# Kernel tuning notes

Hardware: AMD Instinct MI355X
Metric: run time of the kernel (lower is better)

Reference implementation:

```python
import jax, jax.numpy as jnp
import numpy as np

N = 100000
E = 1600000
F_IN = 512
H1, C1 = 8, 8      # layer-1: 8 heads, 8 dims each (concat -> 64)
H2, C2 = 1, 16     # layer-2: 1 head, num_classes=16
SLOPE = 0.2        # GATConv leaky_relu negative slope


def setup_inputs() -> dict:
    key = jax.random.key(0)
    ks = jax.random.split(key, 10)
    x = jax.random.normal(ks[0], (N, F_IN), dtype=jnp.float32)
    edge_index = jax.random.randint(ks[1], (2, E), 0, N, dtype=jnp.int32)
    s = 0.05
    W1 = jax.random.normal(ks[2], (F_IN, H1 * C1), dtype=jnp.float32) * s
    a1_src = jax.random.normal(ks[3], (H1, C1), dtype=jnp.float32) * s
    a1_dst = jax.random.normal(ks[4], (H1, C1), dtype=jnp.float32) * s
    b1 = jnp.zeros((H1 * C1,), dtype=jnp.float32)
    W2 = jax.random.normal(ks[5], (H1 * C1, H2 * C2), dtype=jnp.float32) * s
    a2_src = jax.random.normal(ks[6], (H2, C2), dtype=jnp.float32) * s
    a2_dst = jax.random.normal(ks[7], (H2, C2), dtype=jnp.float32) * s
    b2 = jnp.zeros((H2 * C2,), dtype=jnp.float32)
    return {"x": x, "edge_index": edge_index, "W1": W1, "a1_src": a1_src,
            "a1_dst": a1_dst, "b1": b1, "W2": W2, "a2_src": a2_src,
            "a2_dst": a2_dst, "b2": b2}


def _gat_conv(h, src, dst, W, a_src, a_dst, b, heads, ch):
    n = h.shape[0]
    hp = (h @ W).reshape(n, heads, ch)                      # [N,H,C]
    al_s = jnp.einsum('nhc,hc->nh', hp, a_src)              # [N,H]
    al_d = jnp.einsum('nhc,hc->nh', hp, a_dst)              # [N,H]
    e = jax.nn.leaky_relu(al_s[src] + al_d[dst], SLOPE)     # [E,H]
    # segment softmax over edges sharing a destination (self-loops guarantee >=1 edge/node)
    emax = jax.lax.stop_gradient(jax.ops.segment_max(e, dst, num_segments=n))
    ee = jnp.exp(e - emax[dst])
    denom = jax.ops.segment_sum(ee, dst, num_segments=n)
    alpha = ee / denom[dst]                                 # [E,H]
    msg = hp[src] * alpha[:, :, None]                       # [E,H,C]
    out = jax.ops.segment_sum(msg, dst, num_segments=n)     # [N,H,C]
    return out.reshape(n, heads * ch) + b


def reference(x, edge_index, W1, a1_src, a1_dst, b1, W2, a2_src, a2_dst, b2):
    n = x.shape[0]
    loops = jnp.arange(n, dtype=edge_index.dtype)           # add_self_loops=True
    src = jnp.concatenate([edge_index[0], loops])
    dst = jnp.concatenate([edge_index[1], loops])
    h = jax.nn.elu(_gat_conv(x, src, dst, W1, a1_src, a1_dst, b1, H1, C1))
    h = _gat_conv(h, src, dst, W2, a2_src, a2_dst, b2, H2, C2)
    return jax.nn.log_softmax(h, axis=1)
```

## Files before the change

### kernel.cpp

```cpp
#include <hip/hip_runtime.h>
#include <hip/hip_bf16.h>

#define N_NODES 100000
#define F_IN    512
#define H1      8
#define C1      8
#define D1      64
#define C2      16
#define SLOPE   0.2f
#define CAP     48
#define PSHIFT  9
#define PPART   196
#define CAPP    9216
#define CHUNK   4096

__global__ __launch_bounds__(256) void part_kernel(
    const int* __restrict__ ei, int* __restrict__ pcnt, int2* __restrict__ pfifo,
    int E, int total)
{
    __shared__ int hist[PPART];
    __shared__ int lofs[PPART];
    __shared__ int gbase[PPART];
    __shared__ int cursor[PPART];
    __shared__ int sdata[256];
    __shared__ int2 fifo[CHUNK];

    const int t = threadIdx.x;
    const int chunk0 = (int)blockIdx.x * CHUNK;

    for (int i = t; i < PPART; i += 256) hist[i] = 0;
    __syncthreads();

    int srcs[16], dsts[16];
    const int e0 = chunk0 + t * 16;
    if (e0 + 16 <= E) {
#pragma unroll
        for (int q = 0; q < 4; ++q) {
            int4 s = *(const int4*)(ei + e0 + q * 4);
            int4 d = *(const int4*)(ei + E + e0 + q * 4);
            srcs[q*4+0]=s.x; srcs[q*4+1]=s.y; srcs[q*4+2]=s.z; srcs[q*4+3]=s.w;
            dsts[q*4+0]=d.x; dsts[q*4+1]=d.y; dsts[q*4+2]=d.z; dsts[q*4+3]=d.w;
        }
    } else {
#pragma unroll
        for (int j = 0; j < 16; ++j) {
            int e = e0 + j;
            if (e < E)          { srcs[j] = ei[e]; dsts[j] = ei[E + e]; }
            else if (e < total) { srcs[j] = dsts[j] = e - E; }
            else                { srcs[j] = -1;    dsts[j] = -1; }
        }
    }
#pragma unroll
    for (int j = 0; j < 16; ++j)
        if (dsts[j] >= 0) atomicAdd(&hist[dsts[j] >> PSHIFT], 1);
    __syncthreads();

    int hv = (t < PPART) ? hist[t] : 0;
    sdata[t] = hv;
    __syncthreads();
    for (int off = 1; off < 256; off <<= 1) {
        int x = (t >= off) ? sdata[t - off] : 0;
        __syncthreads();
        sdata[t] += x;
        __syncthreads();
    }
    if (t < PPART) {
        int lo = sdata[t] - hv;
        lofs[t]   = lo;
        cursor[t] = lo;
        gbase[t]  = hv ? atomicAdd(&pcnt[t], hv) : 0;
    }
    __syncthreads();

#pragma unroll
    for (int j = 0; j < 16; ++j) {
        if (dsts[j] >= 0) {
            int p = dsts[j] >> PSHIFT;
            int slot = atomicAdd(&cursor[p], 1);
            fifo[slot] = make_int2(srcs[j], dsts[j]);
        }
    }
    __syncthreads();

    const int w = t >> 6, lane = t & 63;
    for (int p = w; p < PPART; p += 4) {
        int len = hist[p];
        int lo  = lofs[p];
        int gb  = gbase[p];
        int2* dstp = pfifo + (size_t)p * CAPP;
        for (int j = lane; j < len; j += 64) {
            int g = gb + j;
            if (g < CAPP) dstp[g] = fifo[lo + j];
        }
    }
}

__global__ __launch_bounds__(256) void place_kernel(
    const int2* __restrict__ pfifo, const int* __restrict__ pcnt,
    int* __restrict__ buckets, int* __restrict__ cnt, int n)
{
    __shared__ int lcnt[1 << PSHIFT];
    const int p = blockIdx.x;
    const int dbase = p << PSHIFT;
    const int nd = min(1 << PSHIFT, n - dbase);
    const int t = threadIdx.x;
    for (int i = t; i < nd; i += 256) lcnt[i] = 0;
    __syncthreads();

    int len = pcnt[p]; if (len > CAPP) len = CAPP;
    const int2* f = pfifo + (size_t)p * CAPP;

    int i = t;
    for (; i + 768 < len; i += 1024) {
        int2 e0 = f[i], e1 = f[i + 256], e2 = f[i + 512], e3 = f[i + 768];
        int s0 = atomicAdd(&lcnt[e0.y - dbase], 1);
        int s1 = atomicAdd(&lcnt[e1.y - dbase], 1);
        int s2 = atomicAdd(&lcnt[e2.y - dbase], 1);
        int s3 = atomicAdd(&lcnt[e3.y - dbase], 1);
        if (s0 < CAP) buckets[(size_t)e0.y * CAP + s0] = e0.x;
        if (s1 < CAP) buckets[(size_t)e1.y * CAP + s1] = e1.x;
        if (s2 < CAP) buckets[(size_t)e2.y * CAP + s2] = e2.x;
        if (s3 < CAP) buckets[(size_t)e3.y * CAP + s3] = e3.x;
    }
    for (; i < len; i += 256) {
        int2 e = f[i];
        int s = atomicAdd(&lcnt[e.y - dbase], 1);
        if (s < CAP) buckets[(size_t)e.y * CAP + s] = e.x;
    }
    __syncthreads();
    for (int i2 = t; i2 < nd; i2 += 256) cnt[dbase + i2] = min(lcnt[i2], CAP);
}

__global__ __launch_bounds__(256) void gemm1_kernel(
    const float* __restrict__ X, const float* __restrict__ W,
    const float* __restrict__ a1s, const float* __restrict__ a1d,
    float* __restrict__ HP, float* __restrict__ als1, float* __restrict__ ald1,
    int n)
{
    __shared__ float As[16][68];
    __shared__ float Bs[16][68];

    const int t = threadIdx.x;
    const int rowbase = blockIdx.x * 64;
    const int m0 = (t >> 4) << 2;
    const int n0 = (t & 15) << 2;

    const int lr = t >> 2;
    const int lk = (t & 3) << 2;
    const int bk = t >> 4;
    const int bn = (t & 15) << 2;

    const bool arow_ok = (rowbase + lr) < n;
    const float* xrow = X + (size_t)(rowbase + lr) * F_IN;

    float acc[4][4] = {};

    for (int k0 = 0; k0 < F_IN; k0 += 16) {
        float4 av = arow_ok ? *(const float4*)(xrow + k0 + lk)
                            : make_float4(0.f, 0.f, 0.f, 0.f);
        float4 bv = *(const float4*)(W + (size_t)(k0 + bk) * D1 + bn);
        __syncthreads();
        As[lk + 0][lr] = av.x;
        As[lk + 1][lr] = av.y;
        As[lk + 2][lr] = av.z;
        As[lk + 3][lr] = av.w;
        *(float4*)&Bs[bk][bn] = bv;
        __syncthreads();
#pragma unroll
        for (int k = 0; k < 16; ++k) {
            float4 a = *(const float4*)&As[k][m0];
            float4 b = *(const float4*)&Bs[k][n0];
            acc[0][0] += a.x * b.x; acc[0][1] += a.x * b.y; acc[0][2] += a.x * b.z; acc[0][3] += a.x * b.w;
            acc[1][0] += a.y * b.x; acc[1][1] += a.y * b.y; acc[1][2] += a.y * b.z; acc[1][3] += a.y * b.w;
            acc[2][0] += a.z * b.x; acc[2][1] += a.z * b.y; acc[2][2] += a.z * b.z; acc[2][3] += a.z * b.w;
            acc[3][0] += a.w * b.x; acc[3][1] += a.w * b.y; acc[3][2] += a.w * b.z; acc[3][3] += a.w * b.w;
        }
    }

    const float4 s4 = *(const float4*)(a1s + n0);
    const float4 d4 = *(const float4*)(a1d + n0);
    const int h = (t & 15) >> 1;
    const bool evenlane = ((t & 1) == 0);

#pragma unroll
    for (int i = 0; i < 4; ++i) {
        int r = rowbase + m0 + i;
        bool ok = (r < n);
        if (ok) {
            *(float4*)&HP[(size_t)r * D1 + n0] =
                make_float4(acc[i][0], acc[i][1], acc[i][2], acc[i][3]);
        }
        float rs = acc[i][0]*s4.x + acc[i][1]*s4.y + acc[i][2]*s4.z + acc[i][3]*s4.w;
        float rd = acc[i][0]*d4.x + acc[i][1]*d4.y + acc[i][2]*d4.z + acc[i][3]*d4.w;
        rs += __shfl_xor(rs, 1, 64);
        rd += __shfl_xor(rd, 1, 64);
        if (ok && evenlane) {
            als1[(size_t)r * 8 + h] = rs;
            ald1[(size_t)r * 8 + h] = rd;
        }
    }
}

__global__ __launch_bounds__(256) void agg1_kernel(
    const float* __restrict__ hp1,
    const float* __restrict__ als, const float* __restrict__ ald,
    const int* __restrict__ cnt, const int* __restrict__ buckets,
    const float* __restrict__ b1,
    float* __restrict__ h1, int n)
{
    int node = blockIdx.x * 4 + (threadIdx.x >> 6);
    if (node >= n) return;
    int lane = threadIdx.x & 63;
    int h = lane >> 3;

    int m = cnt[node]; if (m > CAP) m = CAP;
    const int* bp = buckets + (size_t)node * CAP;
    float ad = ald[node * 8 + h];
    float den = 0.f, acc = 0.f;

    int i = 0;
    for (; i + 8 <= m; i += 8) {
        int s0 = bp[i + 0], s1 = bp[i + 1], s2 = bp[i + 2], s3 = bp[i + 3];
        int s4 = bp[i + 4], s5 = bp[i + 5], s6 = bp[i + 6], s7 = bp[i + 7];
        float a0 = als[s0 * 8 + h], a1 = als[s1 * 8 + h];
        float a2 = als[s2 * 8 + h], a3 = als[s3 * 8 + h];
        float a4 = als[s4 * 8 + h], a5 = als[s5 * 8 + h];
        float a6 = als[s6 * 8 + h], a7 = als[s7 * 8 + h];
        float v0 = hp1[(size_t)s0 * D1 + lane];
        float v1 = hp1[(size_t)s1 * D1 + lane];
        float v2 = hp1[(size_t)s2 * D1 + lane];
        float v3 = hp1[(size_t)s3 * D1 + lane];
        float v4 = hp1[(size_t)s4 * D1 + lane];
        float v5 = hp1[(size_t)s5 * D1 + lane];
        float v6 = hp1[(size_t)s6 * D1 + lane];
        float v7 = hp1[(size_t)s7 * D1 + lane];
        float e0 = a0 + ad; e0 = (e0 > 0.f) ? e0 : SLOPE * e0;
        float e1 = a1 + ad; e1 = (e1 > 0.f) ? e1 : SLOPE * e1;
        float e2 = a2 + ad; e2 = (e2 > 0.f) ? e2 : SLOPE * e2;
        float e3 = a3 + ad; e3 = (e3 > 0.f) ? e3 : SLOPE * e3;
        float e4 = a4 + ad; e4 = (e4 > 0.f) ? e4 : SLOPE * e4;
        float e5 = a5 + ad; e5 = (e5 > 0.f) ? e5 : SLOPE * e5;
        float e6 = a6 + ad; e6 = (e6 > 0.f) ? e6 : SLOPE * e6;
        float e7 = a7 + ad; e7 = (e7 > 0.f) ? e7 : SLOPE * e7;
        float w0 = __expf(e0), w1 = __expf(e1), w2 = __expf(e2), w3 = __expf(e3);
        float w4 = __expf(e4), w5 = __expf(e5), w6 = __expf(e6), w7 = __expf(e7);
        den += ((w0 + w1) + (w2 + w3)) + ((w4 + w5) + (w6 + w7));
        acc = fmaf(w0, v0, acc);
        acc = fmaf(w1, v1, acc);
        acc = fmaf(w2, v2, acc);
        acc = fmaf(w3, v3, acc);
        acc = fmaf(w4, v4, acc);
        acc = fmaf(w5, v5, acc);
        acc = fmaf(w6, v6, acc);
        acc = fmaf(w7, v7, acc);
    }
    for (; i < m; ++i) {
        int s = bp[i];
        float e = als[s * 8 + h] + ad;
        e = (e > 0.f) ? e : SLOPE * e;
        float ee = __expf(e);
        den += ee;
        acc = fmaf(ee, hp1[(size_t)s * D1 + lane], acc);
    }
    float v = acc / den + b1[lane];
    v = (v > 0.f) ? v : (__expf(v) - 1.f);
    h1[(size_t)node * D1 + lane] = v;
}

__global__ __launch_bounds__(256) void gemm2_kernel(
    const float* __restrict__ H, const float* __restrict__ W2,
    const float* __restrict__ a2s, const float* __restrict__ a2d,
    float* __restrict__ HP2, float* __restrict__ als2, float* __restrict__ ald2,
    int n)
{
    __shared__ float Ws[64 * 16];
    int t = threadIdx.x;
    for (int i = t; i < 1024; i += 256) Ws[i] = W2[i];
    __syncthreads();
    int idx = blockIdx.x * 256 + t;
    int node = idx >> 4, c = idx & 15;
    if (node >= n) return;
    const float* hr = H + (size_t)node * D1;
    float acc = 0.f;
#pragma unroll 8
    for (int k = 0; k < 64; ++k) acc = fmaf(hr[k], Ws[k * 16 + c], acc);
    HP2[idx] = acc;

    float rs = acc * a2s[c];
    float rd = acc * a2d[c];
    rs += __shfl_xor(rs, 8, 16);  rd += __shfl_xor(rd, 8, 16);
    rs += __shfl_xor(rs, 4, 16);  rd += __shfl_xor(rd, 4, 16);
    rs += __shfl_xor(rs, 2, 16);  rd += __shfl_xor(rd, 2, 16);
    rs += __shfl_xor(rs, 1, 16);  rd += __shfl_xor(rd, 1, 16);
    if (c == 0) { als2[node] = rs; ald2[node] = rd; }
}

__global__ __launch_bounds__(256) void agg2_kernel(
    const float* __restrict__ hp2,
    const float* __restrict__ als, const float* __restrict__ ald,
    const int* __restrict__ cnt, const int* __restrict__ buckets,
    const float* __restrict__ b2,
    float* __restrict__ out, int n)
{
    int node = blockIdx.x * 16 + (threadIdx.x >> 4);
    if (node >= n) return;
    int c = threadIdx.x & 15;

    int m0c = cnt[node]; if (m0c > CAP) m0c = CAP;
    const int* bp = buckets + (size_t)node * CAP;
    float ad = ald[node];
    float den = 0.f, acc = 0.f;

    int i = 0;
    for (; i + 8 <= m0c; i += 8) {
        int s0 = bp[i + 0], s1 = bp[i + 1], s2 = bp[i + 2], s3 = bp[i + 3];
        int s4 = bp[i + 4], s5 = bp[i + 5], s6 = bp[i + 6], s7 = bp[i + 7];
        float a0 = als[s0], a1 = als[s1], a2 = als[s2], a3 = als[s3];
        float a4 = als[s4], a5 = als[s5], a6 = als[s6], a7 = als[s7];
        float v0 = hp2[(size_t)s0 * 16 + c];
        float v1 = hp2[(size_t)s1 * 16 + c];
        float v2 = hp2[(size_t)s2 * 16 + c];
        float v3 = hp2[(size_t)s3 * 16 + c];
        float v4 = hp2[(size_t)s4 * 16 + c];
        float v5 = hp2[(size_t)s5 * 16 + c];
        float v6 = hp2[(size_t)s6 * 16 + c];
        float v7 = hp2[(size_t)s7 * 16 + c];
        float e0 = a0 + ad; e0 = (e0 > 0.f) ? e0 : SLOPE * e0;
        float e1 = a1 + ad; e1 = (e1 > 0.f) ? e1 : SLOPE * e1;
        float e2 = a2 + ad; e2 = (e2 > 0.f) ? e2 : SLOPE * e2;
        float e3 = a3 + ad; e3 = (e3 > 0.f) ? e3 : SLOPE * e3;
        float e4 = a4 + ad; e4 = (e4 > 0.f) ? e4 : SLOPE * e4;
        float e5 = a5 + ad; e5 = (e5 > 0.f) ? e5 : SLOPE * e5;
        float e6 = a6 + ad; e6 = (e6 > 0.f) ? e6 : SLOPE * e6;
        float e7 = a7 + ad; e7 = (e7 > 0.f) ? e7 : SLOPE * e7;
        float w0 = __expf(e0), w1 = __expf(e1), w2 = __expf(e2), w3 = __expf(e3);
        float w4 = __expf(e4), w5 = __expf(e5), w6 = __expf(e6), w7 = __expf(e7);
        den += ((w0 + w1) + (w2 + w3)) + ((w4 + w5) + (w6 + w7));
        acc = fmaf(w0, v0, acc);
        acc = fmaf(w1, v1, acc);
        acc = fmaf(w2, v2, acc);
        acc = fmaf(w3, v3, acc);
        acc = fmaf(w4, v4, acc);
        acc = fmaf(w5, v5, acc);
        acc = fmaf(w6, v6, acc);
        acc = fmaf(w7, v7, acc);
    }
    for (; i < m0c; ++i) {
        int s = bp[i];
        float e = als[s] + ad;
        e = (e > 0.f) ? e : SLOPE * e;
        float ee = __expf(e);
        den += ee;
        acc = fmaf(ee, hp2[(size_t)s * 16 + c], acc);
    }
    float v = acc / den + b2[c];

    float m = v;
    m = fmaxf(m, __shfl_xor(m, 8, 16));
    m = fmaxf(m, __shfl_xor(m, 4, 16));
    m = fmaxf(m, __shfl_xor(m, 2, 16));
    m = fmaxf(m, __shfl_xor(m, 1, 16));
    float ex = __expf(v - m);
    float sum = ex;
    sum += __shfl_xor(sum, 8, 16);
    sum += __shfl_xor(sum, 4, 16);
    sum += __shfl_xor(sum, 2, 16);
    sum += __shfl_xor(sum, 1, 16);
    out[(size_t)node * 16 + c] = v - m - __logf(sum);
}

extern "C" void kernel_launch(void* const* d_in, const int* in_sizes, int n_in,
                              void* d_out, int out_size, void* d_ws, size_t ws_size,
                              hipStream_t stream)
{
    const float* x      = (const float*)d_in[0];
    const int*   ei     = (const int*)  d_in[1];
    const float* W1     = (const float*)d_in[2];
    const float* a1_src = (const float*)d_in[3];
    const float* a1_dst = (const float*)d_in[4];
    const float* b1     = (const float*)d_in[5];
    const float* W2     = (const float*)d_in[6];
    const float* a2_src = (const float*)d_in[7];
    const float* a2_dst = (const float*)d_in[8];
    const float* b2     = (const float*)d_in[9];
    float* out = (float*)d_out;

    const int N = in_sizes[0] / F_IN;
    const int E = in_sizes[1] / 2;
    const int TOT = E + N;

    char* base = (char*)d_ws;
    size_t off = 0;
    auto carve = [&](size_t bytes) -> char* {
        char* p = base + off;
        off += (bytes + 255) & ~(size_t)255;
        return p;
    };
    float* hp1     = (float*)carve((size_t)N * D1 * 4);
    float* h1      = (float*)carve((size_t)N * D1 * 4);
    float* hp2     = (float*)carve((size_t)N * 16 * 4);
    float* als1    = (float*)carve((size_t)N * 8 * 4);
    float* ald1    = (float*)carve((size_t)N * 8 * 4);
    float* als2    = (float*)carve((size_t)N * 4);
    float* ald2    = (float*)carve((size_t)N * 4);
    int*   cnt     = (int*)  carve((size_t)N * 4);
    int*   pcnt    = (int*)  carve((size_t)PPART * 4);
    int*   buckets = (int*)  carve((size_t)N * CAP * 4);
    int2*  pfifo   = (int2*)h1;

    const int Gp = (TOT + CHUNK - 1) / CHUNK;

    hipMemsetAsync(pcnt, 0, (size_t)PPART * 4, stream);

    part_kernel<<<Gp, 256, 0, stream>>>(ei, pcnt, pfifo, E, TOT);
    place_kernel<<<PPART, 256, 0, stream>>>(pfifo, pcnt, buckets, cnt, N);

    gemm1_kernel<<<(N + 63) / 64, 256, 0, stream>>>(x, W1, a1_src, a1_dst,
                                                    hp1, als1, ald1, N);

    agg1_kernel<<<(N + 3) / 4, 256, 0, stream>>>(hp1, als1, ald1, cnt, buckets, b1, h1, N);

    gemm2_kernel<<<(N * 16 + 255) / 256, 256, 0, stream>>>(h1, W2, a2_src, a2_dst, hp2, als2, ald2, N);

    agg2_kernel<<<(N + 15) / 16, 256, 0, stream>>>(hp2, als2, ald2, cnt, buckets, b2, out, N);
}
```

Measured before the change: 526.4 us.

## Use bf16 MFMA for layer-1 projection GEMM with pre-transposed bf16 weights

Rewrites the first GEMM (X @ W1, 100000x512x64) to convert X to bf16 on the fly and run it on MFMA 16x16x32 bf16 instructions instead of fp32 FMA outer products. A small kernel transposes and converts W1 to bf16 on each call, and the attention-logit reductions are redone with lane shuffles matched to the MFMA output layout. This removes the FMA-bound compute of the GEMM and leaves it limited by the fp32 X read. It loses precision from bf16 rounding of the inputs and adds one extra launch.

```diff
diff --git a/kernel.cpp b/kernel.cpp
--- a/kernel.cpp
+++ b/kernel.cpp
@@ -14,6 +14,19 @@
 #define CAPP    9216
 #define CHUNK   4096
 
+typedef __bf16 bf16_t;
+typedef bf16_t bf16x8 __attribute__((ext_vector_type(8)));
+typedef float  f32x4  __attribute__((ext_vector_type(4)));
+
+__global__ __launch_bounds__(256) void wcvt_kernel(
+    const float* __restrict__ W, bf16_t* __restrict__ Bt)
+{
+    int i = blockIdx.x * 256 + threadIdx.x;
+    if (i >= 64 * 512) return;
+    int nn = i >> 9, k = i & 511;
+    Bt[i] = (bf16_t)W[k * 64 + nn];
+}
+
 __global__ __launch_bounds__(256) void part_kernel(
     const int* __restrict__ ei, int* __restrict__ pcnt, int2* __restrict__ pfifo,
     int E, int total)
@@ -132,71 +145,110 @@
 }
 
 __global__ __launch_bounds__(256) void gemm1_kernel(
-    const float* __restrict__ X, const float* __restrict__ W,
+    const float* __restrict__ X, const bf16_t* __restrict__ Bt,
     const float* __restrict__ a1s, const float* __restrict__ a1d,
     float* __restrict__ HP, float* __restrict__ als1, float* __restrict__ ald1,
     int n)
 {
-    __shared__ float As[16][68];
-    __shared__ float Bs[16][68];
+    __shared__ __align__(16) bf16_t Asm[4096];
+    __shared__ __align__(16) bf16_t Bsm[4096];
 
     const int t = threadIdx.x;
-    const int rowbase = blockIdx.x * 64;
-    const int m0 = (t >> 4) << 2;
-    const int n0 = (t & 15) << 2;
-
-    const int lr = t >> 2;
-    const int lk = (t & 3) << 2;
-    const int bk = t >> 4;
-    const int bn = (t & 15) << 2;
-
-    const bool arow_ok = (rowbase + lr) < n;
-    const float* xrow = X + (size_t)(rowbase + lr) * F_IN;
-
-    float acc[4][4] = {};
-
-    for (int k0 = 0; k0 < F_IN; k0 += 16) {
-        float4 av = arow_ok ? *(const float4*)(xrow + k0 + lk)
-                            : make_float4(0.f, 0.f, 0.f, 0.f);
-        float4 bv = *(const float4*)(W + (size_t)(k0 + bk) * D1 + bn);
+    const int rowbase = (int)blockIdx.x * 64;
+    const int wave = t >> 6;
+    const int lane = t & 63;
+
+    const int srow  = t >> 2;
+    const int skloc = (t & 3) * 16;
+
+    const int grow = rowbase + srow;
+    const bool rok = grow < n;
+    const float*  xrow = X  + (size_t)grow * F_IN;
+    const bf16_t* brow = Bt + (size_t)srow * F_IN;
+
+    int offA[2];
+#pragma unroll
+    for (int u = 0; u < 2; ++u) {
+        int kloc = skloc + u * 8;
+        int s    = kloc >> 5;
+        int quad = (kloc >> 3) & 3;
+        offA[u] = s * 2048 + (((srow >> 4) * 64) + quad * 16 + (srow & 15)) * 8;
+    }
+
+    f32x4 acc[4];
+#pragma unroll
+    for (int nt = 0; nt < 4; ++nt) acc[nt] = (f32x4){0.f, 0.f, 0.f, 0.f};
+
+    for (int k0 = 0; k0 < F_IN; k0 += 64) {
+        float4 xa0, xa1, xa2, xa3;
+        if (rok) {
+            xa0 = *(const float4*)(xrow + k0 + skloc + 0);
+            xa1 = *(const float4*)(xrow + k0 + skloc + 4);
+            xa2 = *(const float4*)(xrow + k0 + skloc + 8);
+            xa3 = *(const float4*)(xrow + k0 + skloc + 12);
+        } else {
+            xa0 = xa1 = xa2 = xa3 = make_float4(0.f, 0.f, 0.f, 0.f);
+        }
+        bf16x8 bb0 = *(const bf16x8*)(brow + k0 + skloc);
+        bf16x8 bb1 = *(const bf16x8*)(brow + k0 + skloc + 8);
+
         __syncthreads();
-        As[lk + 0][lr] = av.x;
-        As[lk + 1][lr] = av.y;
-        As[lk + 2][lr] = av.z;
-        As[lk + 3][lr] = av.w;
-        *(float4*)&Bs[bk][bn] = bv;
+
+        bf16x8 af0, af1;
+        af0[0]=(bf16_t)xa0.x; af0[1]=(bf16_t)xa0.y; af0[2]=(bf16_t)xa0.z; af0[3]=(bf16_t)xa0.w;
+        af0[4]=(bf16_t)xa1.x; af0[5]=(bf16_t)xa1.y; af0[6]=(bf16_t)xa1.z; af0[7]=(bf16_t)xa1.w;
+        af1[0]=(bf16_t)xa2.x; af1[1]=(bf16_t)xa2.y; af1[2]=(bf16_t)xa2.z; af1[3]=(bf16_t)xa2.w;
+        af1[4]=(bf16_t)xa3.x; af1[5]=(bf16_t)xa3.y; af1[6]=(bf16_t)xa3.z; af1[7]=(bf16_t)xa3.w;
+        *(bf16x8*)(Asm + offA[0]) = af0;
+        *(bf16x8*)(Asm + offA[1]) = af1;
+        *(bf16x8*)(Bsm + offA[0]) = bb0;
+        *(bf16x8*)(Bsm + offA[1]) = bb1;
+
         __syncthreads();
-#pragma unroll
-        for (int k = 0; k < 16; ++k) {
-            float4 a = *(const float4*)&As[k][m0];
-            float4 b = *(const float4*)&Bs[k][n0];
-            acc[0][0] += a.x * b.x; acc[0][1] += a.x * b.y; acc[0][2] += a.x * b.z; acc[0][3] += a.x * b.w;
-            acc[1][0] += a.y * b.x; acc[1][1] += a.y * b.y; acc[1][2] += a.y * b.z; acc[1][3] += a.y * b.w;
-            acc[2][0] += a.z * b.x; acc[2][1] += a.z * b.y; acc[2][2] += a.z * b.z; acc[2][3] += a.z * b.w;
-            acc[3][0] += a.w * b.x; acc[3][1] += a.w * b.y; acc[3][2] += a.w * b.z; acc[3][3] += a.w * b.w;
-        }
-    }
-
-    const float4 s4 = *(const float4*)(a1s + n0);
-    const float4 d4 = *(const float4*)(a1d + n0);
-    const int h = (t & 15) >> 1;
-    const bool evenlane = ((t & 1) == 0);
+
+#pragma unroll
+        for (int s = 0; s < 2; ++s) {
+            bf16x8 a = *(const bf16x8*)(Asm + s * 2048 + (wave * 64 + lane) * 8);
+#pragma unroll
+            for (int nt = 0; nt < 4; ++nt) {
+                bf16x8 b = *(const bf16x8*)(Bsm + s * 2048 + (nt * 64 + lane) * 8);
+                acc[nt] = __builtin_amdgcn_mfma_f32_16x16x32_bf16(a, b, acc[nt], 0, 0, 0);
+            }
+        }
+    }
+
+    const int colg = lane & 15;
+    const int quad = lane >> 4;
+    const int b    = colg >> 3;
+    float cs[4], cd[4];
+#pragma unroll
+    for (int nt = 0; nt < 4; ++nt) {
+        cs[nt] = a1s[nt * 16 + colg];
+        cd[nt] = a1d[nt * 16 + colg];
+    }
 
 #pragma unroll
     for (int i = 0; i < 4; ++i) {
-        int r = rowbase + m0 + i;
-        bool ok = (r < n);
+        int r = rowbase + wave * 16 + quad * 4 + i;
+        bool ok = r < n;
         if (ok) {
-            *(float4*)&HP[(size_t)r * D1 + n0] =
-                make_float4(acc[i][0], acc[i][1], acc[i][2], acc[i][3]);
-        }
-        float rs = acc[i][0]*s4.x + acc[i][1]*s4.y + acc[i][2]*s4.z + acc[i][3]*s4.w;
-        float rd = acc[i][0]*d4.x + acc[i][1]*d4.y + acc[i][2]*d4.z + acc[i][3]*d4.w;
-        rs += __shfl_xor(rs, 1, 64);
-        rd += __shfl_xor(rd, 1, 64);
-        if (ok && evenlane) {
-            als1[(size_t)r * 8 + h] = rs;
-            ald1[(size_t)r * 8 + h] = rd;
+            float* hr = HP + (size_t)r * D1;
+            hr[colg]      = acc[0][i];
+            hr[16 + colg] = acc[1][i];
+            hr[32 + colg] = acc[2][i];
+            hr[48 + colg] = acc[3][i];
+        }
+#pragma unroll
+        for (int nt = 0; nt < 4; ++nt) {
+            float ps = acc[nt][i] * cs[nt];
+            float pd = acc[nt][i] * cd[nt];
+            ps += __shfl_xor(ps, 1, 64);  pd += __shfl_xor(pd, 1, 64);
+            ps += __shfl_xor(ps, 2, 64);  pd += __shfl_xor(pd, 2, 64);
+            ps += __shfl_xor(ps, 4, 64);  pd += __shfl_xor(pd, 4, 64);
+            if (ok && (colg & 7) == 0) {
+                als1[(size_t)r * 8 + 2 * nt + b] = ps;
+                ald1[(size_t)r * 8 + 2 * nt + b] = pd;
+            }
         }
     }
 }
@@ -396,26 +448,28 @@
         off += (bytes + 255) & ~(size_t)255;
         return p;
     };
-    float* hp1     = (float*)carve((size_t)N * D1 * 4);
-    float* h1      = (float*)carve((size_t)N * D1 * 4);
-    float* hp2     = (float*)carve((size_t)N * 16 * 4);
-    float* als1    = (float*)carve((size_t)N * 8 * 4);
-    float* ald1    = (float*)carve((size_t)N * 8 * 4);
-    float* als2    = (float*)carve((size_t)N * 4);
-    float* ald2    = (float*)carve((size_t)N * 4);
-    int*   cnt     = (int*)  carve((size_t)N * 4);
-    int*   pcnt    = (int*)  carve((size_t)PPART * 4);
-    int*   buckets = (int*)  carve((size_t)N * CAP * 4);
+    float*  hp1     = (float*) carve((size_t)N * D1 * 4);
+    float*  h1      = (float*) carve((size_t)N * D1 * 4);
+    float*  hp2     = (float*) carve((size_t)N * 16 * 4);
+    float*  als1    = (float*) carve((size_t)N * 8 * 4);
+    float*  ald1    = (float*) carve((size_t)N * 8 * 4);
+    float*  als2    = (float*) carve((size_t)N * 4);
+    float*  ald2    = (float*) carve((size_t)N * 4);
+    int*    cnt     = (int*)   carve((size_t)N * 4);
+    int*    pcnt    = (int*)   carve((size_t)PPART * 4);
+    int*    buckets = (int*)   carve((size_t)N * CAP * 4);
+    bf16_t* W1b     = (bf16_t*)carve((size_t)64 * 512 * 2);
     int2*  pfifo   = (int2*)h1;
 
     const int Gp = (TOT + CHUNK - 1) / CHUNK;
 
     hipMemsetAsync(pcnt, 0, (size_t)PPART * 4, stream);
 
+    wcvt_kernel<<<128, 256, 0, stream>>>(W1, W1b);
     part_kernel<<<Gp, 256, 0, stream>>>(ei, pcnt, pfifo, E, TOT);
     place_kernel<<<PPART, 256, 0, stream>>>(pfifo, pcnt, buckets, cnt, N);
 
-    gemm1_kernel<<<(N + 63) / 64, 256, 0, stream>>>(x, W1, a1_src, a1_dst,
+    gemm1_kernel<<<(N + 63) / 64, 256, 0, stream>>>(x, W1b, a1_src, a1_dst,
                                                     hp1, als1, ald1, N);
 
     agg1_kernel<<<(N + 3) / 4, 256, 0, stream>>>(hp1, als1, ald1, cnt, buckets, b1, h1, N);
```

Measured after the change: 522.9 us. About the same (-0.7%).
